# Performance work log

Hardware: AMD Instinct MI355X
Metric: run time of the kernel (lower is better)

Reference implementation:

```python
import jax, jax.numpy as jnp
import numpy as np

B, CIN, COUT, K, L = 32, 128, 128, 7, 4096
STRIDE, PAD = 1, 3
TEMP = 1.0


def setup_inputs() -> dict:
    key = jax.random.key(0)
    k1, k2 = jax.random.split(key)
    x = jax.random.normal(k1, (B, CIN, L), dtype=jnp.float32)
    weight = jax.random.normal(k2, (COUT, CIN, K), dtype=jnp.float32) * 0.1  # init: normal(0, 0.1)
    bias = jnp.zeros((COUT,), dtype=jnp.float32)
    return {"x": x, "weight": weight, "bias": bias}


def reference(x, weight, bias):
    # Soft tropical conv (intended math of the module):
    #   y[b,o,w] = T * logsumexp_{c,k}( (x[b,c,w*stride+k] + W[o,c,k]) / T ) + bias[o]
    # with -inf padding (exp(-inf)=0 => plain zero padding in exp space).
    # Computed as a numerically-stabilized standard conv in exp space, which is
    # mathematically identical and avoids materializing the (B,O,C,K,L) tensor.
    xm = jnp.max(x)
    wm = jnp.max(weight)
    ex = jnp.exp((x - xm) / TEMP)          # (B, CIN, L)
    ew = jnp.exp((weight - wm) / TEMP)     # (COUT, CIN, K)
    s = jax.lax.conv_general_dilated(
        ex, ew,
        window_strides=(STRIDE,),
        padding=[(PAD, PAD)],
        dimension_numbers=("NCH", "OIH", "NCH"),
    )  # (B, COUT, L_out); cross-correlation, matching torch unfold indexing x[i+k]
    y = TEMP * jnp.log(s) + (xm + wm)
    return y + bias[None, :, None]
```

## Files before the change

### kernel.cpp

```cpp
#include <hip/hip_runtime.h>
#include <hip/hip_bf16.h>
#include <cstdint>
#include <cstddef>

#define B_N   32
#define CIN_  128
#define COUT_ 128
#define KW_   7
#define L_    4096
#define PAD_  3
#define NW_   128
#define BC_   32
#define RPB   4104
#define NWELEM (KW_ * COUT_ * CIN_)
#define NGUARD (B_N * 8 * CIN_)

#define SW_ELEMS (KW_ * COUT_ * BC_)
#define SX_ROWS  192
#define SX_ELEMS (SX_ROWS * BC_)
#define NGRAN_W  (SW_ELEMS / 8)
#define NGRAN_T  ((SW_ELEMS + SX_ELEMS) / 8)

typedef __attribute__((ext_vector_type(8))) short  bf16x8;
typedef __attribute__((ext_vector_type(4))) float  f32x4;

__device__ __forceinline__ void gl2lds16(const void* g, void* l) {
    __builtin_amdgcn_global_load_lds(
        (const __attribute__((address_space(1))) unsigned int*)g,
        (__attribute__((address_space(3))) unsigned int*)l, 16, 0, 0);
}

__global__ void prep_wg_kernel(const float* __restrict__ w,
                               __hip_bfloat16* __restrict__ ewb,
                               __hip_bfloat16* __restrict__ exT) {
    int idx = blockIdx.x * 256 + threadIdx.x;
    if (idx < NWELEM) {
        int c = idx & 127, rest = idx >> 7;
        int o = rest & 127, k = rest >> 7;
        ewb[idx] = __float2bfloat16(__expf(w[(o * CIN_ + c) * KW_ + k]));
    } else if (idx < NWELEM + NGUARD) {
        int j  = idx - NWELEM;
        int b  = j >> 10, rr = (j >> 7) & 7, c = j & 127;
        int r  = (rr < 3) ? rr : (4096 + rr);
        exT[((size_t)b * RPB + r) * CIN_ + c] = __float2bfloat16(0.0f);
    }
}

__global__ __launch_bounds__(256) void exp_x_kernel(
        const float* __restrict__ x, __hip_bfloat16* __restrict__ exT) {
    __shared__ __align__(16) __hip_bfloat16 tileT[64 * 136];
    const int b  = blockIdx.y;
    const int l0 = blockIdx.x * 64;
    const int tid = threadIdx.x;
    const float* xb = x + (size_t)b * CIN_ * L_ + l0;

    #pragma unroll
    for (int i = 0; i < 8; ++i) {
        int idx = tid + 256 * i;
        int c   = idx >> 4;
        int lv4 = (idx & 15) * 4;
        f32x4 v = *(const f32x4*)(xb + (size_t)c * L_ + lv4);
        #pragma unroll
        for (int k2 = 0; k2 < 4; ++k2) {
            int l  = lv4 + k2;
            int sw = (l >> 2) & 15;
            tileT[l * 136 + (c ^ (sw << 3))] = __float2bfloat16(__expf(v[k2]));
        }
    }
    __syncthreads();

    __hip_bfloat16* dst = exT + ((size_t)b * RPB + l0 + PAD_) * CIN_;
    #pragma unroll
    for (int i = 0; i < 4; ++i) {
        int idx = tid + 256 * i;
        int l  = idx >> 4;
        int gc = idx & 15;
        int sw = (l >> 2) & 15;
        bf16x8 vv = *(const bf16x8*)&tileT[l * 136 + ((gc ^ sw) << 3)];
        *(bf16x8*)(dst + (size_t)l * CIN_ + gc * 8) = vv;
    }
}

__global__ __launch_bounds__(256, 2) void tropconv_kernel(
        const __hip_bfloat16* __restrict__ exT,
        const __hip_bfloat16* __restrict__ ewb,
        const float* __restrict__ bias,
        float* __restrict__ out) {
    __shared__ __align__(16) __hip_bfloat16 smem[SW_ELEMS + SX_ELEMS];
    __hip_bfloat16* sW = smem;
    __hip_bfloat16* sX = smem + SW_ELEMS;

    const int tid  = threadIdx.x;
    const int lane = tid & 63;
    const int wave = tid >> 6;
    const int wm   = wave >> 1;
    const int wn   = wave & 1;
    const int l15  = lane & 15;
    const int q    = lane >> 4;

    const int b  = blockIdx.y;
    const int w0 = blockIdx.x * NW_;
    const __hip_bfloat16* exb = exT + ((size_t)b * RPB + w0) * CIN_;

    f32x4 acc[4][4];
    #pragma unroll
    for (int i = 0; i < 4; ++i)
        #pragma unroll
        for (int j = 0; j < 4; ++j)
            acc[i][j] = (f32x4){0.f, 0.f, 0.f, 0.f};

    for (int c = 0; c < 4; ++c) {
        const int c0 = c * BC_;

        #pragma unroll
        for (int s = 0; s < 17; ++s) {
            int g = tid + 256 * s;
            if (g < NGRAN_W) {
                int row = g >> 2, j = g & 3;
                gl2lds16(ewb + ((size_t)row << 7) + c0 + j * 8, &sW[g * 8]);
            } else {
                int gx = g - NGRAN_W;
                int p = gx >> 2, j = gx & 3;
                gl2lds16(exb + ((size_t)p << 7) + c0 + j * 8, &sX[gx * 8]);
            }
        }
        __syncthreads();

        #pragma unroll
        for (int t = 0; t < KW_; ++t) {
            bf16x8 af[4], bx[4];
            #pragma unroll
            for (int mi = 0; mi < 4; ++mi) {
                int o = wm * 64 + mi * 16 + l15;
                af[mi] = *(const bf16x8*)&sW[(t * COUT_ + o) * BC_ + q * 8];
            }
            #pragma unroll
            for (int ni = 0; ni < 4; ++ni) {
                int p = wn * 64 + ni * 16 + l15 + t;
                bx[ni] = *(const bf16x8*)&sX[p * BC_ + q * 8];
            }
            #pragma unroll
            for (int mi = 0; mi < 4; ++mi)
                #pragma unroll
                for (int ni = 0; ni < 4; ++ni)
                    acc[mi][ni] = __builtin_amdgcn_mfma_f32_16x16x32_bf16(
                        af[mi], bx[ni], acc[mi][ni], 0, 0, 0);
        }
        __syncthreads();
    }

    float* outb = out + (size_t)b * COUT_ * L_;
    #pragma unroll
    for (int mi = 0; mi < 4; ++mi) {
        #pragma unroll
        for (int r = 0; r < 4; ++r) {
            int o = wm * 64 + mi * 16 + q * 4 + r;
            float bv = bias[o];
            #pragma unroll
            for (int ni = 0; ni < 4; ++ni) {
                int w = w0 + wn * 64 + ni * 16 + l15;
                outb[(size_t)o * L_ + w] = __logf(acc[mi][ni][r]) + bv;
            }
        }
    }
}

extern "C" void kernel_launch(void* const* d_in, const int* in_sizes, int n_in,
                              void* d_out, int out_size, void* d_ws, size_t ws_size,
                              hipStream_t stream) {
    const float* x    = (const float*)d_in[0];
    const float* wgt  = (const float*)d_in[1];
    const float* bias = (const float*)d_in[2];
    float* out = (float*)d_out;

    __hip_bfloat16* exT = (__hip_bfloat16*)d_ws;
    __hip_bfloat16* ewb = (__hip_bfloat16*)((char*)d_ws + (size_t)B_N * RPB * CIN_ * 2);

    prep_wg_kernel<<<(NWELEM + NGUARD + 255) / 256, 256, 0, stream>>>(wgt, ewb, exT);
    exp_x_kernel<<<dim3(L_ / 64, B_N), 256, 0, stream>>>(x, exT);
    tropconv_kernel<<<dim3(L_ / NW_, B_N), 256, 0, stream>>>(exT, ewb, bias, out);
}
```

Baseline: 149.7 us.

## Widen conv output tile, swizzle LDS layouts, fuse prep into exp kernel

Doubles the per-block output width to 256 positions so each wave holds a 4x8 accumulator tile, which reuses each weight fragment across more MFMAs and loads less halo per output. The weight LDS layout is reordered into MFMA-fragment order and the x tile gets an XOR swizzle, both aimed at cutting LDS bank conflicts. The weight-exp and guard-zero prep kernel is merged into the exp_x launch as extra blocks, removing one kernel launch. The larger tile raises register pressure and LDS use, which may reduce occupancy under launch_bounds(256,2), and halves the grid to 512 blocks.

```diff
diff --git a/kernel.cpp b/kernel.cpp
--- a/kernel.cpp
+++ b/kernel.cpp
@@ -9,14 +9,14 @@
 #define KW_   7
 #define L_    4096
 #define PAD_  3
-#define NW_   128
+#define NW_   256
 #define BC_   32
 #define RPB   4104
 #define NWELEM (KW_ * COUT_ * CIN_)
 #define NGUARD (B_N * 8 * CIN_)
 
 #define SW_ELEMS (KW_ * COUT_ * BC_)
-#define SX_ROWS  192
+#define SX_ROWS  320
 #define SX_ELEMS (SX_ROWS * BC_)
 #define NGRAN_W  (SW_ELEMS / 8)
 #define NGRAN_T  ((SW_ELEMS + SX_ELEMS) / 8)
@@ -30,24 +30,29 @@
         (__attribute__((address_space(3))) unsigned int*)l, 16, 0, 0);
 }
 
-__global__ void prep_wg_kernel(const float* __restrict__ w,
-                               __hip_bfloat16* __restrict__ ewb,
-                               __hip_bfloat16* __restrict__ exT) {
-    int idx = blockIdx.x * 256 + threadIdx.x;
-    if (idx < NWELEM) {
-        int c = idx & 127, rest = idx >> 7;
-        int o = rest & 127, k = rest >> 7;
-        ewb[idx] = __float2bfloat16(__expf(w[(o * CIN_ + c) * KW_ + k]));
-    } else if (idx < NWELEM + NGUARD) {
-        int j  = idx - NWELEM;
-        int b  = j >> 10, rr = (j >> 7) & 7, c = j & 127;
-        int r  = (rr < 3) ? rr : (4096 + rr);
-        exT[((size_t)b * RPB + r) * CIN_ + c] = __float2bfloat16(0.0f);
+__global__ __launch_bounds__(256) void exp_x_kernel(
+        const float* __restrict__ x, __hip_bfloat16* __restrict__ exT,
+        const float* __restrict__ w, __hip_bfloat16* __restrict__ ewb) {
+    if (blockIdx.x >= 64) {
+        if (blockIdx.y != 0) return;
+        int base = (blockIdx.x - 64) * 256 + threadIdx.x;
+        #pragma unroll
+        for (int i = 0; i < 32; ++i) {
+            int idx = base + 4608 * i;
+            if (idx < NWELEM) {
+                int c = idx & 127, rest = idx >> 7;
+                int o = rest & 127, k = rest >> 7;
+                ewb[idx] = __float2bfloat16(__expf(w[(o * CIN_ + c) * KW_ + k]));
+            } else {
+                int j  = idx - NWELEM;
+                int b  = j >> 10, rr = (j >> 7) & 7, c = j & 127;
+                int r  = (rr < 3) ? rr : (4096 + rr);
+                exT[((size_t)b * RPB + r) * CIN_ + c] = __float2bfloat16(0.0f);
+            }
+        }
+        return;
     }
-}
 
-__global__ __launch_bounds__(256) void exp_x_kernel(
-        const float* __restrict__ x, __hip_bfloat16* __restrict__ exT) {
     __shared__ __align__(16) __hip_bfloat16 tileT[64 * 136];
     const int b  = blockIdx.y;
     const int l0 = blockIdx.x * 64;
@@ -88,7 +93,7 @@
         float* __restrict__ out) {
     __shared__ __align__(16) __hip_bfloat16 smem[SW_ELEMS + SX_ELEMS];
     __hip_bfloat16* sW = smem;
-    __hip_bfloat16* sX = smem + SW_ELEMS;
+    __hip_bfloat16* sX = smem + SX_ELEMS == nullptr ? nullptr : smem + SW_ELEMS;
 
     const int tid  = threadIdx.x;
     const int lane = tid & 63;
@@ -102,47 +107,50 @@
     const int w0 = blockIdx.x * NW_;
     const __hip_bfloat16* exb = exT + ((size_t)b * RPB + w0) * CIN_;
 
-    f32x4 acc[4][4];
+    f32x4 acc[4][8];
     #pragma unroll
     for (int i = 0; i < 4; ++i)
         #pragma unroll
-        for (int j = 0; j < 4; ++j)
+        for (int j = 0; j < 8; ++j)
             acc[i][j] = (f32x4){0.f, 0.f, 0.f, 0.f};
 
     for (int c = 0; c < 4; ++c) {
         const int c0 = c * BC_;
 
         #pragma unroll
-        for (int s = 0; s < 17; ++s) {
-            int g = tid + 256 * s;
-            if (g < NGRAN_W) {
-                int row = g >> 2, j = g & 3;
-                gl2lds16(ewb + ((size_t)row << 7) + c0 + j * 8, &sW[g * 8]);
-            } else {
-                int gx = g - NGRAN_W;
-                int p = gx >> 2, j = gx & 3;
-                gl2lds16(exb + ((size_t)p << 7) + c0 + j * 8, &sX[gx * 8]);
-            }
+        for (int s = 0; s < 14; ++s) {
+            int g  = tid + 256 * s;
+            int li = g & 63;
+            int blk = g >> 6;
+            int t  = blk >> 3;
+            int og = blk & 7;
+            gl2lds16(ewb + ((((t << 7) + (og << 4) + (li & 15)) << 7) + c0 + ((li >> 4) << 3)),
+                     &sW[g * 8]);
+        }
+        #pragma unroll
+        for (int s = 0; s < 5; ++s) {
+            int gx = tid + 256 * s;
+            int p  = gx >> 2, j = gx & 3;
+            int cj = j ^ ((p >> 1) & 3);
+            gl2lds16(exb + ((size_t)p << 7) + c0 + (cj << 3), &sX[gx * 8]);
         }
         __syncthreads();
 
         #pragma unroll
         for (int t = 0; t < KW_; ++t) {
-            bf16x8 af[4], bx[4];
+            bf16x8 af[4], bx[8];
             #pragma unroll
-            for (int mi = 0; mi < 4; ++mi) {
-                int o = wm * 64 + mi * 16 + l15;
-                af[mi] = *(const bf16x8*)&sW[(t * COUT_ + o) * BC_ + q * 8];
-            }
+            for (int mi = 0; mi < 4; ++mi)
+                af[mi] = *(const bf16x8*)&sW[((t * 8 + wm * 4 + mi) << 9) + lane * 8];
             #pragma unroll
-            for (int ni = 0; ni < 4; ++ni) {
-                int p = wn * 64 + ni * 16 + l15 + t;
-                bx[ni] = *(const bf16x8*)&sX[p * BC_ + q * 8];
+            for (int ni = 0; ni < 8; ++ni) {
+                int p = wn * 128 + ni * 16 + l15 + t;
+                bx[ni] = *(const bf16x8*)&sX[(p << 5) + ((q ^ ((p >> 1) & 3)) << 3)];
             }
             #pragma unroll
             for (int mi = 0; mi < 4; ++mi)
                 #pragma unroll
-                for (int ni = 0; ni < 4; ++ni)
+                for (int ni = 0; ni < 8; ++ni)
                     acc[mi][ni] = __builtin_amdgcn_mfma_f32_16x16x32_bf16(
                         af[mi], bx[ni], acc[mi][ni], 0, 0, 0);
         }
@@ -157,8 +165,8 @@
             int o = wm * 64 + mi * 16 + q * 4 + r;
             float bv = bias[o];
             #pragma unroll
-            for (int ni = 0; ni < 4; ++ni) {
-                int w = w0 + wn * 64 + ni * 16 + l15;
+            for (int ni = 0; ni < 8; ++ni) {
+                int w = w0 + wn * 128 + ni * 16 + l15;
                 outb[(size_t)o * L_ + w] = __logf(acc[mi][ni][r]) + bv;
             }
         }
@@ -176,7 +184,6 @@
     __hip_bfloat16* exT = (__hip_bfloat16*)d_ws;
     __hip_bfloat16* ewb = (__hip_bfloat16*)((char*)d_ws + (size_t)B_N * RPB * CIN_ * 2);
 
-    prep_wg_kernel<<<(NWELEM + NGUARD + 255) / 256, 256, 0, stream>>>(wgt, ewb, exT);
-    exp_x_kernel<<<dim3(L_ / 64, B_N), 256, 0, stream>>>(x, exT);
+    exp_x_kernel<<<dim3(64 + 18, B_N), 256, 0, stream>>>(x, exT, wgt, ewb);
     tropconv_kernel<<<dim3(L_ / NW_, B_N), 256, 0, stream>>>(exT, ewb, bias, out);
 }
```

Result: no change. 146.8 us (-1.9%).
